# Kernel optimization log

Measured on AMD Instinct MI355X. Metric: run time of the kernel, lower is better.

The kernel has to match this reference:

```python
import jax, jax.numpy as jnp
import numpy as np

N_OBJ = 8        # objects per sample -> nc2 = 28 pair-nodes per sample (code caps nc2 < 30)
MAX_REL = 10     # relations per sample (num_rel is uniform so total_rels is static)


def setup_inputs() -> dict:
    key = jax.random.key(0)
    k1, k2, k3, k4, k5 = jax.random.split(key, 5)
    B, D, n = 1024, 512, N_OBJ
    iu, ju = np.triu_indices(n, k=1)                     # (i<j) pair layout, lexicographic
    nc2 = iu.shape[0]                                     # 28
    bcol = np.repeat(np.arange(B), nc2)
    slicing_tensor = jnp.asarray(
        np.stack([bcol, np.tile(iu, B), np.tile(ju, B)], axis=1), dtype=jnp.int32)  # [B*nc2, 3]
    spatial_branch_feature_map = jax.random.normal(k1, (B * nc2, D), dtype=jnp.float32)
    W_self = jax.random.normal(k2, (D, D), dtype=jnp.float32) / np.float32(np.sqrt(D))
    W_nbr = jax.random.normal(k3, (D, D), dtype=jnp.float32) / np.float32(np.sqrt(D))
    b = jnp.zeros((D,), dtype=jnp.float32)
    # object_pairs: distinct indices in [0, n)
    i0 = jax.random.randint(k4, (B, MAX_REL), 0, n)
    off = jax.random.randint(k5, (B, MAX_REL), 1, n)
    i1 = (i0 + off) % n
    object_pairs = jnp.stack([i0, i1], axis=-1).astype(jnp.int32)  # [B, MAX_REL, 2]
    num_rel = jnp.full((B,), MAX_REL, dtype=jnp.int32)
    num_obj = jnp.full((B,), n, dtype=jnp.int32)
    return {"spatial_branch_feature_map": spatial_branch_feature_map, "W_self": W_self,
            "W_nbr": W_nbr, "b": b, "slicing_tensor": slicing_tensor,
            "object_pairs": object_pairs, "num_rel": num_rel, "num_obj": num_obj}


def reference(spatial_branch_feature_map, W_self, W_nbr, b,
              slicing_tensor, object_pairs, num_rel, num_obj):
    x = spatial_branch_feature_map
    N, D = x.shape
    B = num_obj.shape[0]
    nc2 = N // B                                          # pair-nodes per sample
    n = N_OBJ
    # --- fully-connected edge index per sample (incl. self-loops), offset per batch ---
    src_l = jnp.repeat(jnp.arange(nc2, dtype=jnp.int32), nc2)   # row0: t1 outer loop
    dst_l = jnp.tile(jnp.arange(nc2, dtype=jnp.int32), nc2)     # row1: t2 inner loop
    offs = (jnp.arange(B, dtype=jnp.int32) * nc2)[:, None]
    src = (src_l[None, :] + offs).reshape(-1)                   # [B*nc2^2]
    dst = (dst_l[None, :] + offs).reshape(-1)
    # --- GNN layer: sum-aggregate neighbor messages, linear + ReLU ---
    agg = jax.ops.segment_sum(x[src], dst, num_segments=N)      # [N, D]
    h = jax.nn.relu(x @ W_self + agg @ W_nbr + b)               # [N, D]
    # --- key-matching gather (replaces nested python-loop boolean matching) ---
    keys = slicing_tensor[:, 0] * (n * n) + slicing_tensor[:, 1] * n + slicing_tensor[:, 2]
    lut = jnp.zeros((B * n * n,), dtype=jnp.int32).at[keys].set(jnp.arange(N, dtype=jnp.int32))
    pmin = jnp.minimum(object_pairs[..., 0], object_pairs[..., 1])
    pmax = jnp.maximum(object_pairs[..., 0], object_pairs[..., 1])
    bidx = jnp.arange(B, dtype=jnp.int32)[:, None]
    rel_keys = (bidx * (n * n) + pmin * n + pmax).reshape(-1)   # [B*MAX_REL]
    rows = lut[rel_keys]
    return h[rows]                                              # [total_rels, D]
```

## Files before the change

### kernel.cpp

```cpp
#include <hip/hip_runtime.h>
#include <hip/hip_bf16.h>
#include <stdint.h>


typedef __bf16 bf16_t;
typedef __bf16 bf16x8 __attribute__((ext_vector_type(8)));
typedef __bf16 bf16x4 __attribute__((ext_vector_type(4)));
typedef float  f32x4  __attribute__((ext_vector_type(4)));

#define D_DIM 512
#define NC2   28
#define NOBJ  8
#define MAXREL 10
#define B_SAMP 1024
#define OUTROWS (B_SAMP * MAXREL)

__device__ __forceinline__ void gload_lds16(const void* g, void* l) {
  __builtin_amdgcn_global_load_lds(
      (const __attribute__((address_space(1))) unsigned int*)g,
      (__attribute__((address_space(3))) unsigned int*)l, 16, 0, 0);
}

__global__ __launch_bounds__(256) void prep_kernel(
    const float* __restrict__ x, const float* __restrict__ Wself,
    const float* __restrict__ Wnbr, const int* __restrict__ pairs,
    bf16_t* __restrict__ Sbf, bf16_t* __restrict__ Abf,
    bf16_t* __restrict__ Wsf, bf16_t* __restrict__ Wnf)
{
  const int blk = blockIdx.x, tid = threadIdx.x;
  if (blk < B_SAMP) {
    __shared__ int rel_row[MAXREL];
    __shared__ float4 oddsum[128];
    if (tid < MAXREL) {
      int p0 = pairs[blk * MAXREL * 2 + tid * 2 + 0];
      int p1 = pairs[blk * MAXREL * 2 + tid * 2 + 1];
      int pmin = min(p0, p1), pmax = max(p0, p1);
      rel_row[tid] = 7 * pmin - (pmin * (pmin - 1)) / 2 + (pmax - pmin - 1);
    }
    __syncthreads();

    const int h = tid >> 7, c = tid & 127;
    const float4* x4 = (const float4*)(x + (size_t)blk * NC2 * D_DIM);
    float4 a = {0.f, 0.f, 0.f, 0.f};
    #pragma unroll
    for (int rp = 0; rp < NC2 / 2; ++rp) {
      float4 v = x4[(rp * 2 + h) * 128 + c];
      a.x += v.x; a.y += v.y; a.z += v.z; a.w += v.w;
    }
    if (h) oddsum[c] = a;
    __syncthreads();
    if (!h) {
      float4 b = oddsum[c];
      bf16x4 o = { (bf16_t)(a.x + b.x), (bf16_t)(a.y + b.y),
                   (bf16_t)(a.z + b.z), (bf16_t)(a.w + b.w) };
      *(bf16x4*)(Sbf + (size_t)blk * D_DIM + c * 4) = o;
    }
    #pragma unroll
    for (int j = h; j < MAXREL; j += 2) {
      float4 v = x4[rel_row[j] * 128 + c];
      bf16x4 o = { (bf16_t)v.x, (bf16_t)v.y, (bf16_t)v.z, (bf16_t)v.w };
      *(bf16x4*)(Abf + (size_t)(blk * MAXREL + j) * D_DIM + c * 4) = o;
    }
  } else {
    __shared__ float tile[32 * 33];
    const int r = blk - B_SAMP;
    const float* W  = (r & 256) ? Wnbr : Wself;
    bf16_t*     Wf  = (r & 256) ? Wnf  : Wsf;
    const int piece = r & 255;
    const int tstep = piece & 15, nblk = piece >> 4;
    const int k0 = tstep * 32, n0 = nblk * 32;
    const int tx = tid & 31, ty = tid >> 5;
    #pragma unroll
    for (int i = 0; i < 32; i += 8)
      tile[(ty + i) * 33 + tx] = W[(size_t)(k0 + ty + i) * D_DIM + n0 + tx];
    __syncthreads();
    const int cfl = tid >> 7, rem = tid & 127;
    const int ll = rem >> 1, eh = rem & 1;
    const int kb = (ll >> 4) * 8 + eh * 4;
    const int nl = cfl * 16 + (ll & 15);
    bf16x4 o = { (bf16_t)tile[(kb + 0) * 33 + nl], (bf16_t)tile[(kb + 1) * 33 + nl],
                 (bf16_t)tile[(kb + 2) * 33 + nl], (bf16_t)tile[(kb + 3) * 33 + nl] };
    const int cf = nblk * 2 + cfl;
    *(bf16x4*)(Wf + ((size_t)(cf * 16 + tstep) * 64 + ll) * 8 + eh * 4) = o;
  }
}

#define SA_BYTES 6144

#define DO_STEP(BS, BN) do {                                                  \
    const bf16_t* aC = (const bf16_t*)(pool + cur * SA_BYTES);                \
    bf16x8 af[6];                                                             \
    _Pragma("unroll")                                                         \
    for (int s_ = 0; s_ < 6; ++s_)                                            \
      af[s_] = *(const bf16x8*)(aC + (s_ * 16 + lr) * 32 + xorc);             \
    _Pragma("unroll")                                                         \
    for (int s_ = 0; s_ < 5; ++s_)                                            \
      acc[s_] = __builtin_amdgcn_mfma_f32_16x16x32_bf16(af[s_], BS, acc[s_], 0, 0, 0); \
    acc[5] = __builtin_amdgcn_mfma_f32_16x16x32_bf16(af[5], BN, acc[5], 0, 0, 0); \
  } while (0)

__global__ __launch_bounds__(256, 5) void fused_gemm_kernel(
    const bf16_t* __restrict__ Abf, const bf16_t* __restrict__ Sbf,
    const bf16_t* __restrict__ Wsf, const bf16_t* __restrict__ Wnf,
    const float* __restrict__ bias, float* __restrict__ out)
{
  __shared__ __align__(16) unsigned char pool[2 * SA_BYTES];

  const int tid = threadIdx.x;
  const int w = tid >> 6, l = tid & 63;
  const int kg = l >> 4, lr = l & 15;
  const int n0w = blockIdx.y * 64 + w * 16;
  const int arow0 = blockIdx.x * 80;
  const int srow0 = blockIdx.x * 8;
  const int cf = blockIdx.y * 4 + w;

  const bf16_t* pBs = Wsf + (size_t)cf * 16 * 512 + (size_t)l * 8;
  const bf16_t* pBn = Wnf + (size_t)cf * 16 * 512 + (size_t)l * 8;

  f32x4 acc[6] = {};

  auto STAGE = [&](int bsel, int k0) {
    bf16_t* aB = (bf16_t*)(pool + bsel * SA_BYTES);
    #pragma unroll
    for (int r = 0; r < 2; ++r) {
      int slot = r * 4 + w;
      if (slot < 6) {
        int c = slot * 64 + l;
        int row = c >> 2, ch = c & 3;
        int sch = ch ^ ((row >> 1) & 3);
        const bf16_t* g = (row < 80)
            ? Abf + (size_t)(arow0 + row) * D_DIM + k0 + sch * 8
            : Sbf + (size_t)(srow0 + (row & 7)) * D_DIM + k0 + sch * 8;
        gload_lds16(g, aB + (size_t)c * 8);
      }
    }
  };

  bf16x8 bsX, bnX, bsY, bnY;
  STAGE(0, 0);
  bsX = *(const bf16x8*)(pBs);
  bnX = *(const bf16x8*)(pBn);
  __syncthreads();

  const int xorc = (kg ^ ((lr >> 1) & 3)) * 8;
  int cur = 0;
  #pragma unroll
  for (int t = 0; t < 16; t += 2) {
    if (t + 1 < 16) {
      STAGE(cur ^ 1, (t + 1) * 32);
      bsY = *(const bf16x8*)(pBs + (t + 1) * 512);
      bnY = *(const bf16x8*)(pBn + (t + 1) * 512);
    }
    DO_STEP(bsX, bnX);
    __syncthreads();
    cur ^= 1;

    if (t + 2 < 16) {
      STAGE(cur ^ 1, (t + 2) * 32);
      bsX = *(const bf16x8*)(pBs + (t + 2) * 512);
      bnX = *(const bf16x8*)(pBn + (t + 2) * 512);
    }
    DO_STEP(bsY, bnY);
    __syncthreads();
    cur ^= 1;
  }

  float* Tex = (float*)pool;
  #pragma unroll
  for (int reg = 0; reg < 4; ++reg)
    Tex[(w * 8 + ((kg * 4 + reg) & 7)) * 20 + lr] = acc[5][reg];
  __syncthreads();

  const float bv = bias[n0w + lr];
  #pragma unroll
  for (int s = 0; s < 5; ++s) {
    #pragma unroll
    for (int reg = 0; reg < 4; ++reg) {
      int rloc = s * 16 + kg * 4 + reg;
      int ls = rloc / MAXREL;
      float v = acc[s][reg] + Tex[(w * 8 + ls) * 20 + lr] + bv;
      out[(size_t)(arow0 + rloc) * D_DIM + n0w + lr] = fmaxf(v, 0.0f);
    }
  }
}

extern "C" void kernel_launch(void* const* d_in, const int* in_sizes, int n_in,
                              void* d_out, int out_size, void* d_ws, size_t ws_size,
                              hipStream_t stream) {
  const float* x     = (const float*)d_in[0];
  const float* Wself = (const float*)d_in[1];
  const float* Wnbr  = (const float*)d_in[2];
  const float* bias  = (const float*)d_in[3];
  const int*   pairs = (const int*)d_in[5];

  char* ws = (char*)d_ws;
  size_t off = 0;
  bf16_t* Sbf = (bf16_t*)(ws + off); off += (size_t)B_SAMP * D_DIM * 2;
  bf16_t* Wsf = (bf16_t*)(ws + off); off += (size_t)D_DIM * D_DIM * 2;
  bf16_t* Wnf = (bf16_t*)(ws + off); off += (size_t)D_DIM * D_DIM * 2;
  bf16_t* Abf = (bf16_t*)(ws + off); off += (size_t)OUTROWS * D_DIM * 2;

  prep_kernel<<<B_SAMP + 512, 256, 0, stream>>>(
      x, Wself, Wnbr, pairs, Sbf, Abf, Wsf, Wnf);
  fused_gemm_kernel<<<dim3(OUTROWS / 80, D_DIM / 64), 256, 0, stream>>>(
      Abf, Sbf, Wsf, Wnf, bias, (float*)d_out);
}
```

Measured before the change: 32.71 us.

## Triple-buffer GEMM A-tiles with prefetch depth two and manual vmcnt waits

Switches the fused GEMM main loop from double to triple buffering in LDS, issuing global-to-LDS loads two K-steps ahead. It replaces __syncthreads with explicit s_waitcnt vmcnt counts tuned per wave plus a raw s_barrier, so only the oldest stage must have landed. The aim is to hide more global-load latency behind the MFMAs. The cost is more LDS, occupancy hint lowered from 5 to 4 blocks, and correctness that depends on hand-counted outstanding loads.

```diff
diff --git a/kernel.cpp b/kernel.cpp
--- a/kernel.cpp
+++ b/kernel.cpp
@@ -87,24 +87,12 @@
 
 #define SA_BYTES 6144
 
-#define DO_STEP(BS, BN) do {                                                  \
-    const bf16_t* aC = (const bf16_t*)(pool + cur * SA_BYTES);                \
-    bf16x8 af[6];                                                             \
-    _Pragma("unroll")                                                         \
-    for (int s_ = 0; s_ < 6; ++s_)                                            \
-      af[s_] = *(const bf16x8*)(aC + (s_ * 16 + lr) * 32 + xorc);             \
-    _Pragma("unroll")                                                         \
-    for (int s_ = 0; s_ < 5; ++s_)                                            \
-      acc[s_] = __builtin_amdgcn_mfma_f32_16x16x32_bf16(af[s_], BS, acc[s_], 0, 0, 0); \
-    acc[5] = __builtin_amdgcn_mfma_f32_16x16x32_bf16(af[5], BN, acc[5], 0, 0, 0); \
-  } while (0)
-
-__global__ __launch_bounds__(256, 5) void fused_gemm_kernel(
+__global__ __launch_bounds__(256, 4) void fused_gemm_kernel(
     const bf16_t* __restrict__ Abf, const bf16_t* __restrict__ Sbf,
     const bf16_t* __restrict__ Wsf, const bf16_t* __restrict__ Wnf,
     const float* __restrict__ bias, float* __restrict__ out)
 {
-  __shared__ __align__(16) unsigned char pool[2 * SA_BYTES];
+  __shared__ __align__(16) unsigned char pool[3 * SA_BYTES];
 
   const int tid = threadIdx.x;
   const int w = tid >> 6, l = tid & 63;
@@ -136,34 +124,50 @@
     }
   };
 
-  bf16x8 bsX, bnX, bsY, bnY;
-  STAGE(0, 0);
-  bsX = *(const bf16x8*)(pBs);
-  bnX = *(const bf16x8*)(pBn);
+  const int xorc = (kg ^ ((lr >> 1) & 3)) * 8;
+
+  bf16x8 B0[2], B1[2], B2[2];
+#define LOADB_INTO(BV, t) do {                                                \
+    BV[0] = *(const bf16x8*)(pBs + (t) * 512);                                \
+    BV[1] = *(const bf16x8*)(pBn + (t) * 512);                                \
+  } while (0)
+
+#define DO_STEP(bsel, BV) do {                                                \
+    const bf16_t* aC = (const bf16_t*)(pool + (bsel) * SA_BYTES);             \
+    bf16x8 af[6];                                                             \
+    _Pragma("unroll")                                                         \
+    for (int s_ = 0; s_ < 6; ++s_)                                            \
+      af[s_] = *(const bf16x8*)(aC + (s_ * 16 + lr) * 32 + xorc);             \
+    _Pragma("unroll")                                                         \
+    for (int s_ = 0; s_ < 5; ++s_)                                            \
+      acc[s_] = __builtin_amdgcn_mfma_f32_16x16x32_bf16(af[s_], BV[0], acc[s_], 0, 0, 0); \
+    acc[5] = __builtin_amdgcn_mfma_f32_16x16x32_bf16(af[5], BV[1], acc[5], 0, 0, 0); \
+  } while (0)
+
+  STAGE(0, 0);      LOADB_INTO(B0, 0);
+  STAGE(1, 32);     LOADB_INTO(B1, 1);
+
+#define ITER(t, BCUR, BNXT2) do {                                             \
+    if ((t) == 15)      asm volatile("s_waitcnt vmcnt(0)" ::: "memory");      \
+    else if (w < 2)     asm volatile("s_waitcnt vmcnt(4)" ::: "memory");      \
+    else                asm volatile("s_waitcnt vmcnt(3)" ::: "memory");      \
+    __builtin_amdgcn_s_barrier();                                             \
+    if ((t) + 2 < 16) { STAGE(((t) + 2) % 3, ((t) + 2) * 32);                 \
+                        LOADB_INTO(BNXT2, (t) + 2); }                         \
+    DO_STEP((t) % 3, BCUR);                                                   \
+  } while (0)
+
+  ITER( 0, B0, B2);  ITER( 1, B1, B0);  ITER( 2, B2, B1);
+  ITER( 3, B0, B2);  ITER( 4, B1, B0);  ITER( 5, B2, B1);
+  ITER( 6, B0, B2);  ITER( 7, B1, B0);  ITER( 8, B2, B1);
+  ITER( 9, B0, B2);  ITER(10, B1, B0);  ITER(11, B2, B1);
+  ITER(12, B0, B2);  ITER(13, B1, B0);  ITER(14, B2, B1);
+  ITER(15, B0, B2);
+#undef ITER
+#undef DO_STEP
+#undef LOADB_INTO
+
   __syncthreads();
-
-  const int xorc = (kg ^ ((lr >> 1) & 3)) * 8;
-  int cur = 0;
-  #pragma unroll
-  for (int t = 0; t < 16; t += 2) {
-    if (t + 1 < 16) {
-      STAGE(cur ^ 1, (t + 1) * 32);
-      bsY = *(const bf16x8*)(pBs + (t + 1) * 512);
-      bnY = *(const bf16x8*)(pBn + (t + 1) * 512);
-    }
-    DO_STEP(bsX, bnX);
-    __syncthreads();
-    cur ^= 1;
-
-    if (t + 2 < 16) {
-      STAGE(cur ^ 1, (t + 2) * 32);
-      bsX = *(const bf16x8*)(pBs + (t + 2) * 512);
-      bnX = *(const bf16x8*)(pBn + (t + 2) * 512);
-    }
-    DO_STEP(bsY, bnY);
-    __syncthreads();
-    cur ^= 1;
-  }
 
   float* Tex = (float*)pool;
   #pragma unroll
```

Result: slower. 33.41 us (+2.1%).

## Split GEMM block rows across two wave groups with 512-thread blocks

Applied to the files above, without the earlier changes.

Doubles the GEMM block to 512 threads and splits the 96 staged A rows between two groups of four waves. Each wave now keeps 3 accumulators instead of 6, and the second group handles the neighbor-sum strip. The aim is more waves in flight and lower per-wave register pressure, so global-load latency is hidden better. The cost is more threads issuing redundant B-fragment loads and more threads taking part in each barrier. The strip loop in the epilogue now has a variable trip count.

```diff
diff --git a/kernel.cpp b/kernel.cpp
--- a/kernel.cpp
+++ b/kernel.cpp
@@ -87,19 +87,7 @@
 
 #define SA_BYTES 6144
 
-#define DO_STEP(BS, BN) do {                                                  \
-    const bf16_t* aC = (const bf16_t*)(pool + cur * SA_BYTES);                \
-    bf16x8 af[6];                                                             \
-    _Pragma("unroll")                                                         \
-    for (int s_ = 0; s_ < 6; ++s_)                                            \
-      af[s_] = *(const bf16x8*)(aC + (s_ * 16 + lr) * 32 + xorc);             \
-    _Pragma("unroll")                                                         \
-    for (int s_ = 0; s_ < 5; ++s_)                                            \
-      acc[s_] = __builtin_amdgcn_mfma_f32_16x16x32_bf16(af[s_], BS, acc[s_], 0, 0, 0); \
-    acc[5] = __builtin_amdgcn_mfma_f32_16x16x32_bf16(af[5], BN, acc[5], 0, 0, 0); \
-  } while (0)
-
-__global__ __launch_bounds__(256, 5) void fused_gemm_kernel(
+__global__ __launch_bounds__(512) void fused_gemm_kernel(
     const bf16_t* __restrict__ Abf, const bf16_t* __restrict__ Sbf,
     const bf16_t* __restrict__ Wsf, const bf16_t* __restrict__ Wnf,
     const float* __restrict__ bias, float* __restrict__ out)
@@ -108,77 +96,91 @@
 
   const int tid = threadIdx.x;
   const int w = tid >> 6, l = tid & 63;
+  const int ws = w >> 2, wc = w & 3;
   const int kg = l >> 4, lr = l & 15;
-  const int n0w = blockIdx.y * 64 + w * 16;
+  const int n0w = blockIdx.y * 64 + wc * 16;
   const int arow0 = blockIdx.x * 80;
   const int srow0 = blockIdx.x * 8;
-  const int cf = blockIdx.y * 4 + w;
+  const int cf = blockIdx.y * 4 + wc;
 
   const bf16_t* pBs = Wsf + (size_t)cf * 16 * 512 + (size_t)l * 8;
   const bf16_t* pBn = Wnf + (size_t)cf * 16 * 512 + (size_t)l * 8;
 
-  f32x4 acc[6] = {};
+  f32x4 acc[3] = {};
 
   auto STAGE = [&](int bsel, int k0) {
     bf16_t* aB = (bf16_t*)(pool + bsel * SA_BYTES);
-    #pragma unroll
-    for (int r = 0; r < 2; ++r) {
-      int slot = r * 4 + w;
-      if (slot < 6) {
-        int c = slot * 64 + l;
-        int row = c >> 2, ch = c & 3;
-        int sch = ch ^ ((row >> 1) & 3);
-        const bf16_t* g = (row < 80)
-            ? Abf + (size_t)(arow0 + row) * D_DIM + k0 + sch * 8
-            : Sbf + (size_t)(srow0 + (row & 7)) * D_DIM + k0 + sch * 8;
-        gload_lds16(g, aB + (size_t)c * 8);
-      }
+    if (tid < 384) {
+      int row = tid >> 2, ch = tid & 3;
+      int sch = ch ^ ((row >> 1) & 3);
+      const bf16_t* g = (row < 80)
+          ? Abf + (size_t)(arow0 + row) * D_DIM + k0 + sch * 8
+          : Sbf + (size_t)(srow0 + (row & 7)) * D_DIM + k0 + sch * 8;
+      gload_lds16(g, aB + (size_t)tid * 8);
     }
   };
+
+  const int xorc = (kg ^ ((lr >> 1) & 3)) * 8;
+
+#define LOADB(BS, BN, t) do {                                                 \
+    BS = *(const bf16x8*)(pBs + (t) * 512);                                   \
+    if (ws) BN = *(const bf16x8*)(pBn + (t) * 512);                           \
+  } while (0)
+
+#define DO_STEP(bsel, BS, BN) do {                                            \
+    const bf16_t* aC = (const bf16_t*)(pool + (bsel) * SA_BYTES);             \
+    bf16x8 af[3];                                                             \
+    _Pragma("unroll")                                                         \
+    for (int s_ = 0; s_ < 3; ++s_)                                            \
+      af[s_] = *(const bf16x8*)(aC + ((ws * 48 + s_ * 16) + lr) * 32 + xorc); \
+    acc[0] = __builtin_amdgcn_mfma_f32_16x16x32_bf16(af[0], BS, acc[0], 0, 0, 0); \
+    acc[1] = __builtin_amdgcn_mfma_f32_16x16x32_bf16(af[1], BS, acc[1], 0, 0, 0); \
+    acc[2] = __builtin_amdgcn_mfma_f32_16x16x32_bf16(af[2], ws ? BN : BS, acc[2], 0, 0, 0); \
+  } while (0)
 
   bf16x8 bsX, bnX, bsY, bnY;
   STAGE(0, 0);
-  bsX = *(const bf16x8*)(pBs);
-  bnX = *(const bf16x8*)(pBn);
+  LOADB(bsX, bnX, 0);
   __syncthreads();
 
-  const int xorc = (kg ^ ((lr >> 1) & 3)) * 8;
   int cur = 0;
   #pragma unroll
   for (int t = 0; t < 16; t += 2) {
     if (t + 1 < 16) {
       STAGE(cur ^ 1, (t + 1) * 32);
-      bsY = *(const bf16x8*)(pBs + (t + 1) * 512);
-      bnY = *(const bf16x8*)(pBn + (t + 1) * 512);
-    }
-    DO_STEP(bsX, bnX);
+      LOADB(bsY, bnY, t + 1);
+    }
+    DO_STEP(cur, bsX, bnX);
     __syncthreads();
     cur ^= 1;
 
     if (t + 2 < 16) {
       STAGE(cur ^ 1, (t + 2) * 32);
-      bsX = *(const bf16x8*)(pBs + (t + 2) * 512);
-      bnX = *(const bf16x8*)(pBn + (t + 2) * 512);
-    }
-    DO_STEP(bsY, bnY);
+      LOADB(bsX, bnX, t + 2);
+    }
+    DO_STEP(cur, bsY, bnY);
     __syncthreads();
     cur ^= 1;
   }
+#undef DO_STEP
+#undef LOADB
 
   float* Tex = (float*)pool;
-  #pragma unroll
-  for (int reg = 0; reg < 4; ++reg)
-    Tex[(w * 8 + ((kg * 4 + reg) & 7)) * 20 + lr] = acc[5][reg];
+  if (ws) {
+    #pragma unroll
+    for (int reg = 0; reg < 4; ++reg)
+      Tex[(wc * 8 + ((kg * 4 + reg) & 7)) * 20 + lr] = acc[2][reg];
+  }
   __syncthreads();
 
   const float bv = bias[n0w + lr];
-  #pragma unroll
-  for (int s = 0; s < 5; ++s) {
+  const int nstrips = ws ? 2 : 3;
+  for (int s = 0; s < nstrips; ++s) {
     #pragma unroll
     for (int reg = 0; reg < 4; ++reg) {
-      int rloc = s * 16 + kg * 4 + reg;
+      int rloc = ws * 48 + s * 16 + kg * 4 + reg;
       int ls = rloc / MAXREL;
-      float v = acc[s][reg] + Tex[(w * 8 + ls) * 20 + lr] + bv;
+      float v = acc[s][reg] + Tex[(wc * 8 + ls) * 20 + lr] + bv;
       out[(size_t)(arow0 + rloc) * D_DIM + n0w + lr] = fmaxf(v, 0.0f);
     }
   }
@@ -202,6 +204,6 @@
 
   prep_kernel<<<B_SAMP + 512, 256, 0, stream>>>(
       x, Wself, Wnbr, pairs, Sbf, Abf, Wsf, Wnf);
-  fused_gemm_kernel<<<dim3(OUTROWS / 80, D_DIM / 64), 256, 0, stream>>>(
+  fused_gemm_kernel<<<dim3(OUTROWS / 80, D_DIM / 64), 512, 0, stream>>>(
       Abf, Sbf, Wsf, Wnf, bias, (float*)d_out);
 }
```

Measured after the change: 33.64 us. +2.8%, slower.
